# Optimization experiments

Measured on AMD Instinct MI355X. Metric: run time of the kernel, lower is better.

Reference implementation:

```python
import jax, jax.numpy as jnp
import numpy as np

N, K, D = 256, 16, 1024
EPS = 1e-06


def setup_inputs() -> dict:
    key = jax.random.key(0)
    k1, k2, k3, k4 = jax.random.split(key, 4)
    scale = 0.05  # keep pairwise distances in a non-saturated logit range
    return {
        'image_features': jax.random.normal(k1, (N, K, D), jnp.float32) * scale,
        'caption_features': jax.random.normal(k2, (N, K, D), jnp.float32) * scale,
        'image_logsigma': jax.random.normal(k3, (N, D), jnp.float32),
        'caption_logsigma': jax.random.normal(k4, (N, D), jnp.float32),
        'negative_scale': jnp.full((1,), 5.0, jnp.float32),
        'shift': jnp.full((1,), 5.0, jnp.float32),
    }


def _pairwise_cdist(x, y):
    # dist[i, j, k, l] = || x[i, k] - y[j, l] ||_2, computed via Gram expansion
    # to avoid materializing the (N, N, K, K, D) broadcast-difference tensor.
    x2 = jnp.sum(x * x, axis=-1)  # (N, K)
    y2 = jnp.sum(y * y, axis=-1)  # (N, K)
    xy = jnp.einsum('ikd,jld->ijkl', x, y)  # (N, N, K, K)
    sq = x2[:, None, :, None] + y2[None, :, None, :] - 2.0 * xy
    sq = jnp.maximum(sq, 0.0)
    return jnp.sqrt(sq + EPS)


def _nll_sum(dist, negative_scale, shift):
    # dist: (N, N, K, K) -> logits (N, N, K*K)
    n = dist.shape[0]
    kk = dist.shape[2] * dist.shape[3]
    logits = (-negative_scale[0] * dist + shift[0]).reshape(n, n, kk)
    matched = jnp.where(jnp.eye(n, dtype=bool), 1.0, -1.0)[:, :, None]  # (N, N, 1)
    # logsumexp over the stacked (logit, -logit) pair == logaddexp(l, -l)
    inner = logits * matched - jnp.logaddexp(logits, -logits)
    nll = -jax.scipy.special.logsumexp(inner, axis=-1) + jnp.log(jnp.float32(kk))  # (N, N)
    return jnp.sum(nll)  # pos (diag) + neg (off-diag) sums


def reference(image_features, caption_features, image_logsigma, caption_logsigma,
              negative_scale, shift):
    # uniform_lambda = 0, vib_beta = 0 -> loss = i2t + t2i soft-contrastive NLL
    dist = _pairwise_cdist(image_features, caption_features)  # (N, N, K, K)
    i2t = _nll_sum(dist, negative_scale, shift)
    # t2i: anchors/candidates swapped -> transposed pair grid (same per-pair set)
    t2i = _nll_sum(jnp.transpose(dist, (1, 0, 3, 2)), negative_scale, shift)
    return i2t + t2i
```

## Files before the change

kernel.cpp:

```cpp
#include <hip/hip_runtime.h>
#include <hip/hip_bf16.h>
#include <cstdint>


using f32x4 = __attribute__((ext_vector_type(4))) float;
using s16x8 = __attribute__((ext_vector_type(8))) short;

#define DDIM   1024
#define BM     256
#define BN     256
#define BK     64
#define LOGKK  5.5451774444795625f
#define DEPS   1e-6f

__device__ __forceinline__ void gload16(const void* g, void* l) {
  __builtin_amdgcn_global_load_lds((const __attribute__((address_space(1))) void*)g,
                                   (__attribute__((address_space(3))) void*)l, 16, 0, 0);
}

__device__ __forceinline__ unsigned short bf16_rne(float x) {
  uint32_t u = __builtin_bit_cast(uint32_t, x);
  uint32_t r = (u + 0x7FFFu + ((u >> 16) & 1u)) >> 16;
  return (unsigned short)r;
}

__global__ __launch_bounds__(256) void mcsc_prep(
    const float* __restrict__ img, const float* __restrict__ cap,
    unsigned short* __restrict__ Xhi, unsigned short* __restrict__ Yhi,
    float* __restrict__ x2, float* __restrict__ y2, float* __restrict__ out)
{
  int w = blockIdx.x * 4 + (threadIdx.x >> 6);
  int lane = threadIdx.x & 63;
  int isY = w >> 12;
  int row = w & 4095;
  const float* src = (isY ? cap : img) + (size_t)row * DDIM;
  unsigned short* dst = (isY ? Yhi : Xhi) + (size_t)row * DDIM;

  float s = 0.f;
#pragma unroll
  for (int j = 0; j < 4; ++j) {
    int col = (j * 64 + lane) * 4;
    float4 v = *(const float4*)(src + col);
    const float* vp = (const float*)&v;
    unsigned short h[4];
#pragma unroll
    for (int e = 0; e < 4; ++e) { float x = vp[e]; s += x * x; h[e] = bf16_rne(x); }
    *(ushort4*)(dst + col) = make_ushort4(h[0], h[1], h[2], h[3]);
  }
#pragma unroll
  for (int off = 32; off >= 1; off >>= 1) s += __shfl_xor(s, off);
  if (lane == 0) (isY ? y2 : x2)[row] = s;
  if (w == 0 && lane == 0) out[0] = 0.f;
}

__global__ __launch_bounds__(512, 2) void mcsc_main(
    const unsigned short* __restrict__ Xhi, const unsigned short* __restrict__ Yhi,
    const float* __restrict__ x2, const float* __restrict__ y2,
    const float* __restrict__ nsp, const float* __restrict__ shp,
    float* __restrict__ out)
{
  __shared__ __align__(16) char lds[131072];
  __shared__ float redBuf[8];

  int bid = blockIdx.x;
  int wg = (bid & 7) * 32 + (bid >> 3);
  int bm = wg >> 4, bn = wg & 15;
  int rowBase = bm * BM, colBase = bn * BN;

  int t = threadIdx.x;
  int wid = t >> 6, lane = t & 63;
  int lr = lane & 15, lk = lane >> 4;
  int wr = wid >> 2, wc = wid & 3;
  int waveRow = wr * 128, waveCol = wc * 64;

  f32x4 acc[8][4] = {};

  int srow = wid * 8 + (lane >> 3);
  int scol = (((lane & 7) ^ (lane >> 3)) * 16);
  const char* aPtr[4];
  const char* bPtr[4];
#pragma unroll
  for (int c = 0; c < 4; ++c) {
    aPtr[c] = (const char*)(Xhi + (size_t)(rowBase + c * 64 + srow) * DDIM) + scol;
    bPtr[c] = (const char*)(Yhi + (size_t)(colBase + c * 64 + srow) * DDIM) + scol;
  }
  int ldsDst = wid * 1024;

  auto stage = [&](int ks, int b) {
    int ko = ks * 128;
#pragma unroll
    for (int c = 0; c < 4; ++c) {
      gload16(aPtr[c] + ko, lds + b * 32768 + c * 8192 + ldsDst);
      gload16(bPtr[c] + ko, lds + 65536 + b * 32768 + c * 8192 + ldsDst);
    }
  };

  stage(0, 0);
  __syncthreads();

  for (int ks = 0; ks < 16; ++ks) {
    int cur = ks & 1;
    if (ks < 15) stage(ks + 1, cur ^ 1);

    const char* ldsA = lds + cur * 32768;
    const char* ldsB = lds + 65536 + cur * 32768;
    int swz = (lr & 7) << 4;
#pragma unroll
    for (int kk = 0; kk < BK; kk += 32) {
      int kb = (kk + lk * 8) * 2;
      s16x8 af[8], bf[4];
#pragma unroll
      for (int m = 0; m < 8; ++m) {
        int rl = waveRow + m * 16 + lr;
        af[m] = *(const s16x8*)(ldsA + rl * 128 + (kb ^ swz));
      }
#pragma unroll
      for (int n = 0; n < 4; ++n) {
        int rl = waveCol + n * 16 + lr;
        bf[n] = *(const s16x8*)(ldsB + rl * 128 + (kb ^ swz));
      }
#pragma unroll
      for (int m = 0; m < 8; ++m)
#pragma unroll
        for (int n = 0; n < 4; ++n)
          acc[m][n] = __builtin_amdgcn_mfma_f32_16x16x32_bf16(af[m], bf[n], acc[m][n], 0, 0, 0);
    }
    __syncthreads();
  }

  float ns = nsp[0], sh = shp[0];
  float waveAcc = 0.f;
#pragma unroll
  for (int m = 0; m < 8; ++m) {
    int gr0 = rowBase + waveRow + m * 16;
    f32x4 x2v = *(const f32x4*)(x2 + gr0 + lk * 4);
#pragma unroll
    for (int n = 0; n < 4; ++n) {
      int gc0 = colBase + waveCol + n * 16;
      bool diag = ((gr0 >> 4) == (gc0 >> 4));
      float y2c = y2[gc0 + lr];
      float ts = 0.f;
#pragma unroll
      for (int r = 0; r < 4; ++r) {
        float sq = x2v[r] + y2c - 2.f * acc[m][n][r];
        sq = fmaxf(sq, 0.f);
        float dd = __fsqrt_rn(sq + DEPS);
        float l = sh - ns * dd;
        float a = diag ? (2.f * l) : (-2.f * l);
        ts += 1.f / (1.f + __expf(-a));
      }
#pragma unroll
      for (int off = 32; off >= 1; off >>= 1) ts += __shfl_xor(ts, off);
      waveAcc += (LOGKK - __logf(ts));
    }
  }
  if (lane == 0) redBuf[wid] = waveAcc;
  __syncthreads();
  if (t == 0) {
    float bs = redBuf[0] + redBuf[1] + redBuf[2] + redBuf[3]
             + redBuf[4] + redBuf[5] + redBuf[6] + redBuf[7];
    atomicAdd(out, 2.f * bs);
  }
}

extern "C" void kernel_launch(void* const* d_in, const int* in_sizes, int n_in,
                              void* d_out, int out_size, void* d_ws, size_t ws_size,
                              hipStream_t stream) {
  const float* img = (const float*)d_in[0];
  const float* cap = (const float*)d_in[1];
  const float* nsp = (const float*)d_in[4];
  const float* shp = (const float*)d_in[5];
  float* out = (float*)d_out;

  char* ws = (char*)d_ws;
  unsigned short* Xhi = (unsigned short*)(ws + (size_t)0);
  unsigned short* Yhi = (unsigned short*)(ws + (size_t)8 * 1024 * 1024);
  float* x2 = (float*)(ws + (size_t)16 * 1024 * 1024);
  float* y2 = (float*)(ws + (size_t)16 * 1024 * 1024 + 16384);

  mcsc_prep<<<dim3(2048), dim3(256), 0, stream>>>(img, cap, Xhi, Yhi, x2, y2, out);
  mcsc_main<<<dim3(256), dim3(512), 0, stream>>>(Xhi, Yhi, x2, y2, nsp, shp, out);
}
```

Before: 133.2 us.

## Deepen GEMM pipeline to four LDS stages with smaller K tiles

Switches the main bf16 GEMM loop from a two-buffer BK=64 scheme to a four-slot ring of BK=32 tiles, prefetching three stages ahead. Explicit vmcnt waits and a single barrier per iteration replace the trailing __syncthreads, and the LDS swizzle is reworked for the 64-byte row stride. The aim is to hide global-to-LDS latency better. The cost is twice as many loop iterations with barriers, and the hand-counted vmcnt thresholds are fragile.

New measurement: 139.5 us. +4.7%, slower.

```diff
diff --git a/kernel.cpp b/kernel.cpp
--- a/kernel.cpp
+++ b/kernel.cpp
@@ -9,7 +9,8 @@
 #define DDIM   1024
 #define BM     256
 #define BN     256
-#define BK     64
+#define BK     32
+#define NT     32
 #define LOGKK  5.5451774444795625f
 #define DEPS   1e-6f
 
@@ -59,7 +60,7 @@
     const float* __restrict__ nsp, const float* __restrict__ shp,
     float* __restrict__ out)
 {
-  __shared__ __align__(16) char lds[131072];
+  __shared__ __align__(16) char lds[4 * 32768];
   __shared__ float redBuf[8];
 
   int bid = blockIdx.x;
@@ -75,57 +76,51 @@
 
   f32x4 acc[8][4] = {};
 
-  int srow = wid * 8 + (lane >> 3);
-  int scol = (((lane & 7) ^ (lane >> 3)) * 16);
-  const char* aPtr[4];
-  const char* bPtr[4];
-#pragma unroll
-  for (int c = 0; c < 4; ++c) {
-    aPtr[c] = (const char*)(Xhi + (size_t)(rowBase + c * 64 + srow) * DDIM) + scol;
-    bPtr[c] = (const char*)(Yhi + (size_t)(colBase + c * 64 + srow) * DDIM) + scol;
-  }
+  int srow = wid * 16 + (lane >> 2);
+  int scol = ((lane & 3) ^ ((lane >> 3) & 3)) * 16;
+  const char* aSrc = (const char*)(Xhi + (size_t)(rowBase + srow) * DDIM) + scol;
+  const char* bSrc = (const char*)(Yhi + (size_t)(colBase + srow) * DDIM) + scol;
   int ldsDst = wid * 1024;
 
-  auto stage = [&](int ks, int b) {
-    int ko = ks * 128;
+  auto stage = [&](int ks, int s) {
+    int ko = ks * 64;
+    char* base = lds + s * 32768;
 #pragma unroll
-    for (int c = 0; c < 4; ++c) {
-      gload16(aPtr[c] + ko, lds + b * 32768 + c * 8192 + ldsDst);
-      gload16(bPtr[c] + ko, lds + 65536 + b * 32768 + c * 8192 + ldsDst);
+    for (int i = 0; i < 2; ++i) {
+      gload16(aSrc + (size_t)(i * 128) * 2048 + ko, base + i * 8192 + ldsDst);
+      gload16(bSrc + (size_t)(i * 128) * 2048 + ko, base + 16384 + i * 8192 + ldsDst);
     }
   };
 
-  stage(0, 0);
-  __syncthreads();
+  int rdoff = (lk * 16) ^ (((lr >> 1) & 3) << 4);
+  int aOff = (waveRow + lr) * 64 + rdoff;
+  int bOff = 16384 + (waveCol + lr) * 64 + rdoff;
 
-  for (int ks = 0; ks < 16; ++ks) {
-    int cur = ks & 1;
-    if (ks < 15) stage(ks + 1, cur ^ 1);
+  stage(0, 0); stage(1, 1); stage(2, 2);
 
-    const char* ldsA = lds + cur * 32768;
-    const char* ldsB = lds + 65536 + cur * 32768;
-    int swz = (lr & 7) << 4;
+  for (int ks = 0; ks < NT; ++ks) {
+    int cur = ks & 3;
+    if (ks < NT - 2)       asm volatile("s_waitcnt vmcnt(8)" ::: "memory");
+    else if (ks == NT - 2) asm volatile("s_waitcnt vmcnt(4)" ::: "memory");
+    else                   asm volatile("s_waitcnt vmcnt(0)" ::: "memory");
+    __builtin_amdgcn_s_barrier();
+    __builtin_amdgcn_sched_barrier(0);
+
+    if (ks + 3 < NT) stage(ks + 3, (ks + 3) & 3);
+
+    const char* sBase = lds + cur * 32768;
+    s16x8 af[8], bf[4];
 #pragma unroll
-    for (int kk = 0; kk < BK; kk += 32) {
-      int kb = (kk + lk * 8) * 2;
-      s16x8 af[8], bf[4];
+    for (int m = 0; m < 8; ++m)
+      af[m] = *(const s16x8*)(sBase + aOff + m * 1024);
 #pragma unroll
-      for (int m = 0; m < 8; ++m) {
-        int rl = waveRow + m * 16 + lr;
-        af[m] = *(const s16x8*)(ldsA + rl * 128 + (kb ^ swz));
-      }
+    for (int n = 0; n < 4; ++n)
+      bf[n] = *(const s16x8*)(sBase + bOff + n * 1024);
 #pragma unroll
-      for (int n = 0; n < 4; ++n) {
-        int rl = waveCol + n * 16 + lr;
-        bf[n] = *(const s16x8*)(ldsB + rl * 128 + (kb ^ swz));
-      }
+    for (int m = 0; m < 8; ++m)
 #pragma unroll
-      for (int m = 0; m < 8; ++m)
-#pragma unroll
-        for (int n = 0; n < 4; ++n)
-          acc[m][n] = __builtin_amdgcn_mfma_f32_16x16x32_bf16(af[m], bf[n], acc[m][n], 0, 0, 0);
-    }
-    __syncthreads();
+      for (int n = 0; n < 4; ++n)
+        acc[m][n] = __builtin_amdgcn_mfma_f32_16x16x32_bf16(af[m], bf[n], acc[m][n], 0, 0, 0);
   }
 
   float ns = nsp[0], sh = shp[0];
```
